# Kernel tuning notes

Hardware: AMD Instinct MI355X
Metric: run time of the kernel (lower is better)

## Reference

```python
import jax, jax.numpy as jnp
import numpy as np

NEG_SLOPE = 0.2  # PyG GATConv default LeakyReLU negative slope
NUM_GRAPHS = 256


def gat_conv(x, edge_src, edge_dst, W, att_src, att_dst, bias):
    """PyG-style GATConv. x:[N,Fin], W:[H*C,Fin], att_*:[H,C], bias:[H*C]."""
    N = x.shape[0]
    H, C = att_src.shape
    h = (x @ W.T).reshape(N, H, C)                       # [N,H,C]
    a_src = jnp.sum(h * att_src, axis=-1)                # [N,H]
    a_dst = jnp.sum(h * att_dst, axis=-1)                # [N,H]
    e = jax.nn.leaky_relu(a_src[edge_src] + a_dst[edge_dst], NEG_SLOPE)  # [E,H]
    # segment softmax over edges sharing the same destination node
    m = jax.ops.segment_max(e, edge_dst, num_segments=N)
    ex = jnp.exp(e - m[edge_dst])
    den = jax.ops.segment_sum(ex, edge_dst, num_segments=N)
    alpha = ex / (den[edge_dst] + 1e-16)                 # [E,H]
    out = jax.ops.segment_sum(h[edge_src] * alpha[..., None], edge_dst,
                              num_segments=N)            # [N,H,C]
    return out.reshape(N, H * C) + bias


def setup_inputs() -> dict:
    key = jax.random.key(0)
    ks = jax.random.split(key, 16)
    N, E, Fin = 20000, 320000, 128
    H1, C1 = 8, 64          # conv1: heads=8, hidden_dim1=64 -> concat 512
    D1 = H1 * C1            # 512
    D2 = 128                # hidden_dim2, conv2 heads=1
    OUT = 2
    s = lambda k, shp, fan: jax.random.normal(k, shp, jnp.float32) * (1.0 / np.sqrt(fan))
    x = jax.random.normal(ks[0], (N, Fin), jnp.float32)
    edge_index = jax.random.randint(ks[1], (2, E), 0, N, jnp.int32)
    batch = jnp.sort(jax.random.randint(ks[2], (N,), 0, NUM_GRAPHS, jnp.int32))
    return {
        "x": x, "edge_index": edge_index, "batch": batch,
        "W1": s(ks[3], (D1, Fin), Fin), "att_src1": s(ks[4], (H1, C1), C1),
        "att_dst1": s(ks[5], (H1, C1), C1), "b1": jnp.zeros((D1,), jnp.float32),
        "W2": s(ks[6], (D2, D1), D1), "att_src2": s(ks[7], (1, D2), D2),
        "att_dst2": s(ks[8], (1, D2), D2), "b2": jnp.zeros((D2,), jnp.float32),
        "w_attn": s(ks[9], (D2, 1), D2), "b_attn": jnp.zeros((1,), jnp.float32),
        "w_mask": s(ks[10], (D2, 1), D2), "b_mask": jnp.zeros((1,), jnp.float32),
        "W_out": s(ks[11], (OUT, D2), D2), "b_out": jnp.zeros((OUT,), jnp.float32),
    }


def reference(x, edge_index, batch, W1, att_src1, att_dst1, b1,
              W2, att_src2, att_dst2, b2, w_attn, b_attn, w_mask, b_mask,
              W_out, b_out):
    N = x.shape[0]
    loops = jnp.arange(N, dtype=edge_index.dtype)
    src = jnp.concatenate([edge_index[0], loops])  # PyG add_self_loops=True
    dst = jnp.concatenate([edge_index[1], loops])

    h = gat_conv(x, src, dst, W1, att_src1, att_dst1, b1)   # [N, 512]
    h = jax.nn.relu(h)                                      # dropout = identity (eval)
    h = gat_conv(h, src, dst, W2, att_src2, att_dst2, b2)   # [N, 128]
    h = jax.nn.relu(h)

    # attention pooling over graphs in the batch
    attn_scores = h @ w_attn + b_attn                       # [N,1]
    node_mask = jax.nn.sigmoid(h @ w_mask + b_mask)         # [N,1]
    weighted = h * (attn_scores * node_mask)                # [N,128]
    pooled = jax.ops.segment_sum(weighted, batch, num_segments=NUM_GRAPHS)
    return pooled @ W_out.T + b_out                         # [256, 2]
```

## Files before the change

kernel.cpp:

```cpp
#include <hip/hip_runtime.h>
#include <math.h>


#define NEG_SLOPE 0.2f

using bf16x8 = __attribute__((ext_vector_type(8))) __bf16;
using f32x4  = __attribute__((ext_vector_type(4))) float;

__device__ __forceinline__ ushort f2bf(float f) {
    unsigned u = __float_as_uint(f);
    unsigned r = (u + 0x7FFFu + ((u >> 16) & 1u)) >> 16;
    return (ushort)r;
}
__device__ __forceinline__ unsigned pack2(float a, float b) {
    return (unsigned)f2bf(a) | ((unsigned)f2bf(b) << 16);
}
__device__ __forceinline__ void unpack8(uint4 u, float* f) {
    f[0] = __uint_as_float(u.x << 16); f[1] = __uint_as_float(u.x & 0xFFFF0000u);
    f[2] = __uint_as_float(u.y << 16); f[3] = __uint_as_float(u.y & 0xFFFF0000u);
    f[4] = __uint_as_float(u.z << 16); f[5] = __uint_as_float(u.z & 0xFFFF0000u);
    f[6] = __uint_as_float(u.w << 16); f[7] = __uint_as_float(u.w & 0xFFFF0000u);
}
__device__ __forceinline__ void unpack4(uint2 u, float* f) {
    f[0] = __uint_as_float(u.x << 16); f[1] = __uint_as_float(u.x & 0xFFFF0000u);
    f[2] = __uint_as_float(u.y << 16); f[3] = __uint_as_float(u.y & 0xFFFF0000u);
}

__global__ __launch_bounds__(256) void cvt_bf16(const float* __restrict__ in,
                                                ushort* __restrict__ out, int n4) {
    int i = blockIdx.x * 256 + threadIdx.x;
    if (i >= n4) return;
    float4 v = ((const float4*)in)[i];
    uint2 o;
    o.x = pack2(v.x, v.y);
    o.y = pack2(v.z, v.w);
    ((uint2*)out)[i] = o;
}

__global__ __launch_bounds__(256) void prep_v(const float* __restrict__ W1,
                                              const float* __restrict__ att_s,
                                              const float* __restrict__ att_d,
                                              float* __restrict__ v_s,
                                              float* __restrict__ v_d) {
    int tid = blockIdx.x * 256 + threadIdx.x;
    int h = tid >> 7, f = tid & 127;
    float as = 0.f, ad = 0.f;
    for (int c = 0; c < 64; ++c) {
        float w = W1[(size_t)(h * 64 + c) * 128 + f];
        as += att_s[h * 64 + c] * w;
        ad += att_d[h * 64 + c] * w;
    }
    v_s[tid] = as;
    v_d[tid] = ad;
}

__global__ __launch_bounds__(256) void scoresA(const ushort* __restrict__ xb,
                                               const float* __restrict__ v_s,
                                               const float* __restrict__ v_d,
                                               float* __restrict__ a1s,
                                               float* __restrict__ a1d, int N) {
    int node = blockIdx.x * 4 + (threadIdx.x >> 6);
    if (node >= N) return;
    int lane = threadIdx.x & 63;
    int head = lane >> 3, f0 = (lane & 7) * 16;
    const uint4* xp = (const uint4*)(xb + (size_t)node * 128 + f0);
    float xv[16];
    unpack8(xp[0], xv);
    unpack8(xp[1], xv + 8);
    const float4* sp = (const float4*)(v_s + head * 128 + f0);
    const float4* dp = (const float4*)(v_d + head * 128 + f0);
    float ps = 0.f, pd = 0.f;
#pragma unroll
    for (int q = 0; q < 4; ++q) {
        float4 s4 = sp[q], d4 = dp[q];
        ps += xv[q*4+0]*s4.x + xv[q*4+1]*s4.y + xv[q*4+2]*s4.z + xv[q*4+3]*s4.w;
        pd += xv[q*4+0]*d4.x + xv[q*4+1]*d4.y + xv[q*4+2]*d4.z + xv[q*4+3]*d4.w;
    }
#pragma unroll
    for (int off = 1; off < 8; off <<= 1) {
        ps += __shfl_xor(ps, off);
        pd += __shfl_xor(pd, off);
    }
    if ((lane & 7) == 0) {
        a1s[node * 8 + head] = ps;
        a1d[node * 8 + head] = pd;
    }
}

__global__ void count_edges(const int* __restrict__ dst, int* cnt, int E) {
    int e = blockIdx.x * 256 + threadIdx.x;
    if (e < E) atomicAdd(&cnt[dst[e]], 1);
}

__global__ __launch_bounds__(1024) void scan_offsets(const int* cnt, int* row_start,
                                                     int* cursor, int N) {
    __shared__ int sm[1024];
    int t = threadIdx.x;
    int per = (N + 1023) / 1024;
    int beg = t * per;
    int end = beg + per; if (end > N) end = N;
    int sum = 0;
    for (int i = beg; i < end; ++i) sum += cnt[i];
    sm[t] = sum;
    __syncthreads();
    for (int off = 1; off < 1024; off <<= 1) {
        int add = (t >= off) ? sm[t - off] : 0;
        __syncthreads();
        sm[t] += add;
        __syncthreads();
    }
    int run = sm[t] - sum;
    for (int i = beg; i < end; ++i) {
        int c = cnt[i];
        row_start[i] = run;
        cursor[i] = run;
        run += c;
    }
    if (t == 1023) row_start[N] = run;
}

__global__ void fill_edges(const int* __restrict__ src, const int* __restrict__ dst,
                           int* cursor, int* __restrict__ srcs, int E) {
    int e = blockIdx.x * 256 + threadIdx.x;
    if (e < E) {
        int pos = atomicAdd(&cursor[dst[e]], 1);
        srcs[pos] = src[e];
    }
}

__global__ __launch_bounds__(256) void agg_x(const ushort* __restrict__ xb,
                                             const float* __restrict__ a1s,
                                             const float* __restrict__ a1d,
                                             const int* __restrict__ row_start,
                                             const int* __restrict__ srcs,
                                             ushort* __restrict__ ax, int N) {
    int node = blockIdx.x * 4 + (threadIdx.x >> 6);
    if (node >= N) return;
    int lane = threadIdx.x & 63;
    int head = lane >> 3, f0 = (lane & 7) * 16;
    int pbeg = row_start[node], pend = row_start[node + 1];
    float ad = a1d[node * 8 + head];
    float es = a1s[node * 8 + head] + ad;
    es = es > 0.f ? es : NEG_SLOPE * es;
    float ex_self = __expf(es);
    float den = ex_self;
    float acc[16];
    {
        const uint4* xp = (const uint4*)(xb + (size_t)node * 128 + f0);
        float xv[16];
        unpack8(xp[0], xv);
        unpack8(xp[1], xv + 8);
#pragma unroll
        for (int j = 0; j < 16; ++j) acc[j] = ex_self * xv[j];
    }
    for (int p = pbeg; p < pend; ++p) {
        int s = srcs[p];
        float e = a1s[s * 8 + head] + ad;
        e = e > 0.f ? e : NEG_SLOPE * e;
        float ex = __expf(e);
        den += ex;
        const uint4* xp = (const uint4*)(xb + (size_t)s * 128 + f0);
        float xv[16];
        unpack8(xp[0], xv);
        unpack8(xp[1], xv + 8);
#pragma unroll
        for (int j = 0; j < 16; ++j) acc[j] += ex * xv[j];
    }
    float rden = 1.0f / (den + 1e-16f);
    uint4 o0, o1;
    o0.x = pack2(acc[0] * rden, acc[1] * rden);
    o0.y = pack2(acc[2] * rden, acc[3] * rden);
    o0.z = pack2(acc[4] * rden, acc[5] * rden);
    o0.w = pack2(acc[6] * rden, acc[7] * rden);
    o1.x = pack2(acc[8] * rden, acc[9] * rden);
    o1.y = pack2(acc[10] * rden, acc[11] * rden);
    o1.z = pack2(acc[12] * rden, acc[13] * rden);
    o1.w = pack2(acc[14] * rden, acc[15] * rden);
    uint4* op = (uint4*)(ax + (size_t)node * 1024 + head * 128 + f0);
    op[0] = o0; op[1] = o1;
}

#define LDSB 40
__global__ __launch_bounds__(256) void gemm_grouped(const ushort* __restrict__ AX,
                                                    const ushort* __restrict__ W1b,
                                                    const float* __restrict__ b1,
                                                    ushort* __restrict__ r1,
                                                    int M) {
    __shared__ ushort As[2][128 * LDSB];
    __shared__ ushort Bs[128 * LDSB];
    int t = threadIdx.x;
    int wave = t >> 6, lane = t & 63;
    int quad = lane >> 4, l16 = lane & 15;
    int m0 = blockIdx.x * 128;
    int y = blockIdx.y;
    int wm = (wave & 1) * 64;
    int wn = (wave >> 1) * 64;
    int hsel = wn >> 6;
    int srow = t >> 1;
    int sseg = (t & 1) * 16;
    f32x4 acc[4][4] = {};
    for (int k0 = 0; k0 < 128; k0 += 32) {
        uint4 a0v0, a0v1, a1v0, a1v1, bv0, bv1;
        {
            int grow = m0 + srow;
            if (grow < M) {
                const uint4* g0 = (const uint4*)(AX + (size_t)grow * 1024 + (2 * y) * 128 + k0 + sseg);
                const uint4* g1 = (const uint4*)(AX + (size_t)grow * 1024 + (2 * y + 1) * 128 + k0 + sseg);
                a0v0 = g0[0]; a0v1 = g0[1];
                a1v0 = g1[0]; a1v1 = g1[1];
            } else {
                a0v0 = make_uint4(0, 0, 0, 0); a0v1 = a0v0; a1v0 = a0v0; a1v1 = a0v0;
            }
            const uint4* gq = (const uint4*)(W1b + (size_t)(y * 128 + srow) * 128 + k0 + sseg);
            bv0 = gq[0]; bv1 = gq[1];
        }
        __syncthreads();
        *(uint4*)&As[0][srow * LDSB + sseg]     = a0v0;
        *(uint4*)&As[0][srow * LDSB + sseg + 8] = a0v1;
        *(uint4*)&As[1][srow * LDSB + sseg]     = a1v0;
        *(uint4*)&As[1][srow * LDSB + sseg + 8] = a1v1;
        *(uint4*)&Bs[srow * LDSB + sseg]        = bv0;
        *(uint4*)&Bs[srow * LDSB + sseg + 8]    = bv1;
        __syncthreads();
        bf16x8 af[4], bf[4];
#pragma unroll
        for (int i = 0; i < 4; ++i)
            af[i] = *(const bf16x8*)&As[hsel][(wm + i * 16 + l16) * LDSB + quad * 8];
#pragma unroll
        for (int j = 0; j < 4; ++j)
            bf[j] = *(const bf16x8*)&Bs[(wn + j * 16 + l16) * LDSB + quad * 8];
#pragma unroll
        for (int i = 0; i < 4; ++i)
#pragma unroll
            for (int j = 0; j < 4; ++j)
                acc[i][j] = __builtin_amdgcn_mfma_f32_16x16x32_bf16(
                    af[i], bf[j], acc[i][j], 0, 0, 0);
    }
#pragma unroll
    for (int i = 0; i < 4; ++i) {
#pragma unroll
        for (int r = 0; r < 4; ++r) {
            int grow = m0 + wm + i * 16 + quad * 4 + r;
            if (grow < M) {
#pragma unroll
                for (int j = 0; j < 4; ++j) {
                    int gcol = y * 128 + wn + j * 16 + l16;
                    float v = fmaxf(acc[i][j][r] + b1[gcol], 0.f);
                    r1[(size_t)grow * 512 + gcol] = f2bf(v);
                }
            }
        }
    }
}

__global__ __launch_bounds__(256) void gemm_mfma(const ushort* __restrict__ A,
                                                 const ushort* __restrict__ B,
                                                 ushort* __restrict__ C,
                                                 int M, int N, int K) {
    __shared__ ushort As[128 * LDSB];
    __shared__ ushort Bs[128 * LDSB];
    int t = threadIdx.x;
    int wave = t >> 6, lane = t & 63;
    int quad = lane >> 4, l16 = lane & 15;
    int m0 = blockIdx.x * 128;
    int n0 = blockIdx.y * 128;
    int wm = (wave & 1) * 64;
    int wn = (wave >> 1) * 64;
    int srow = t >> 1;
    int sseg = (t & 1) * 16;
    f32x4 acc[4][4] = {};
    for (int k0 = 0; k0 < K; k0 += 32) {
        uint4 av0, av1, bv0, bv1;
        {
            int grow = m0 + srow;
            if (grow < M) {
                const uint4* gp = (const uint4*)(A + (size_t)grow * K + k0 + sseg);
                av0 = gp[0]; av1 = gp[1];
            } else {
                av0 = make_uint4(0, 0, 0, 0); av1 = av0;
            }
            const uint4* gq = (const uint4*)(B + (size_t)(n0 + srow) * K + k0 + sseg);
            bv0 = gq[0]; bv1 = gq[1];
        }
        __syncthreads();
        *(uint4*)&As[srow * LDSB + sseg]     = av0;
        *(uint4*)&As[srow * LDSB + sseg + 8] = av1;
        *(uint4*)&Bs[srow * LDSB + sseg]     = bv0;
        *(uint4*)&Bs[srow * LDSB + sseg + 8] = bv1;
        __syncthreads();
        bf16x8 af[4], bf[4];
#pragma unroll
        for (int i = 0; i < 4; ++i)
            af[i] = *(const bf16x8*)&As[(wm + i * 16 + l16) * LDSB + quad * 8];
#pragma unroll
        for (int j = 0; j < 4; ++j)
            bf[j] = *(const bf16x8*)&Bs[(wn + j * 16 + l16) * LDSB + quad * 8];
#pragma unroll
        for (int i = 0; i < 4; ++i)
#pragma unroll
            for (int j = 0; j < 4; ++j)
                acc[i][j] = __builtin_amdgcn_mfma_f32_16x16x32_bf16(
                    af[i], bf[j], acc[i][j], 0, 0, 0);
    }
#pragma unroll
    for (int i = 0; i < 4; ++i) {
#pragma unroll
        for (int r = 0; r < 4; ++r) {
            int grow = m0 + wm + i * 16 + quad * 4 + r;
            if (grow < M) {
#pragma unroll
                for (int j = 0; j < 4; ++j) {
                    int gcol = n0 + wn + j * 16 + l16;
                    C[(size_t)grow * N + gcol] = f2bf(acc[i][j][r]);
                }
            }
        }
    }
}

__global__ __launch_bounds__(256) void scores2(const ushort* __restrict__ h2,
                                               const float* __restrict__ att_s,
                                               const float* __restrict__ att_d,
                                               float* __restrict__ a2s,
                                               float* __restrict__ a2d, int N) {
    int node = blockIdx.x * 4 + (threadIdx.x >> 6);
    if (node >= N) return;
    int lane = threadIdx.x & 63;
    unsigned u = *(const unsigned*)(h2 + (size_t)node * 128 + lane * 2);
    float h0 = __uint_as_float(u << 16), h1v = __uint_as_float(u & 0xFFFF0000u);
    float2 s = *(const float2*)(att_s + lane * 2);
    float2 d = *(const float2*)(att_d + lane * 2);
    float ps = h0 * s.x + h1v * s.y;
    float pd = h0 * d.x + h1v * d.y;
#pragma unroll
    for (int off = 1; off < 64; off <<= 1) {
        ps += __shfl_xor(ps, off);
        pd += __shfl_xor(pd, off);
    }
    if (lane == 0) { a2s[node] = ps; a2d[node] = pd; }
}

__global__ __launch_bounds__(256) void agg2pool(const ushort* __restrict__ h2,
                                                const float* __restrict__ a2s,
                                                const float* __restrict__ a2d,
                                                const int* __restrict__ row_start,
                                                const int* __restrict__ srcs,
                                                const float* __restrict__ b2,
                                                const int* __restrict__ batch,
                                                const float* __restrict__ w_attn,
                                                const float* __restrict__ b_attn,
                                                const float* __restrict__ w_mask,
                                                const float* __restrict__ b_mask,
                                                float* pooled, int N) {
    int node = blockIdx.x * 8 + (threadIdx.x >> 5);
    if (node >= N) return;
    int sub = threadIdx.x & 31;
    int f0 = sub * 4;
    int pbeg = row_start[node], pend = row_start[node + 1];
    float ad = a2d[node];
    float es = a2s[node] + ad;
    es = es > 0.f ? es : NEG_SLOPE * es;
    float ex_self = __expf(es);
    float den = ex_self;
    float q[4];
    unpack4(*(const uint2*)(h2 + (size_t)node * 128 + f0), q);
    float acc[4];
#pragma unroll
    for (int j = 0; j < 4; ++j) acc[j] = ex_self * q[j];
    for (int p = pbeg; p < pend; ++p) {
        int s = srcs[p];
        float e = a2s[s] + ad;
        e = e > 0.f ? e : NEG_SLOPE * e;
        float ex = __expf(e);
        den += ex;
        float v[4];
        unpack4(*(const uint2*)(h2 + (size_t)s * 128 + f0), v);
#pragma unroll
        for (int j = 0; j < 4; ++j) acc[j] += ex * v[j];
    }
    float rden = 1.0f / (den + 1e-16f);
    float4 bv = *(const float4*)(b2 + f0);
    float o[4];
    o[0] = fmaxf(acc[0] * rden + bv.x, 0.f);
    o[1] = fmaxf(acc[1] * rden + bv.y, 0.f);
    o[2] = fmaxf(acc[2] * rden + bv.z, 0.f);
    o[3] = fmaxf(acc[3] * rden + bv.w, 0.f);
    float4 wa = *(const float4*)(w_attn + f0);
    float4 wm = *(const float4*)(w_mask + f0);
    float pa = o[0] * wa.x + o[1] * wa.y + o[2] * wa.z + o[3] * wa.w;
    float pm = o[0] * wm.x + o[1] * wm.y + o[2] * wm.z + o[3] * wm.w;
#pragma unroll
    for (int off = 1; off < 32; off <<= 1) {
        pa += __shfl_xor(pa, off);
        pm += __shfl_xor(pm, off);
    }
    float attn = pa + b_attn[0];
    float mask = 1.0f / (1.0f + __expf(-(pm + b_mask[0])));
    float w = attn * mask;
    int g = batch[node];
    float* pp = pooled + g * 128 + f0;
    atomicAdd(pp + 0, o[0] * w);
    atomicAdd(pp + 1, o[1] * w);
    atomicAdd(pp + 2, o[2] * w);
    atomicAdd(pp + 3, o[3] * w);
}

__global__ void final_kernel(const float* __restrict__ pooled,
                             const float* __restrict__ W_out,
                             const float* __restrict__ b_out,
                             float* __restrict__ out) {
    int tid = blockIdx.x * 256 + threadIdx.x;
    if (tid >= 512) return;
    int g = tid >> 1, o = tid & 1;
    const float* p = pooled + g * 128;
    const float* w = W_out + o * 128;
    float s = 0.f;
#pragma unroll 4
    for (int f = 0; f < 128; ++f) s += p[f] * w[f];
    out[tid] = s + b_out[o];
}

extern "C" void kernel_launch(void* const* d_in, const int* in_sizes, int n_in,
                              void* d_out, int out_size, void* d_ws, size_t ws_size,
                              hipStream_t stream) {
    const float* x        = (const float*)d_in[0];
    const int* edge_index = (const int*)d_in[1];
    const int* batch      = (const int*)d_in[2];
    const float* W1       = (const float*)d_in[3];
    const float* att_src1 = (const float*)d_in[4];
    const float* att_dst1 = (const float*)d_in[5];
    const float* b1       = (const float*)d_in[6];
    const float* W2       = (const float*)d_in[7];
    const float* att_src2 = (const float*)d_in[8];
    const float* att_dst2 = (const float*)d_in[9];
    const float* b2       = (const float*)d_in[10];
    const float* w_attn   = (const float*)d_in[11];
    const float* b_attn   = (const float*)d_in[12];
    const float* w_mask   = (const float*)d_in[13];
    const float* b_mask   = (const float*)d_in[14];
    const float* W_out    = (const float*)d_in[15];
    const float* b_out    = (const float*)d_in[16];
    float* out = (float*)d_out;

    int N = in_sizes[0] / 128;
    int E = in_sizes[1] / 2;
    const int* esrc = edge_index;
    const int* edst = edge_index + E;

    char* ws = (char*)d_ws;
    size_t off = 0;
    auto alloc = [&](size_t bytes) {
        void* p = ws + off;
        off = (off + bytes + 255) & ~(size_t)255;
        return p;
    };
    ushort* xb       = (ushort*)alloc((size_t)N * 128 * 2);
    ushort* ax       = (ushort*)alloc((size_t)N * 1024 * 2);
    ushort* r1       = (ushort*)alloc((size_t)N * 512 * 2);
    ushort* h2       = (ushort*)alloc((size_t)N * 128 * 2);
    ushort* w1b      = (ushort*)alloc((size_t)512 * 128 * 2);
    ushort* w2b      = (ushort*)alloc((size_t)128 * 512 * 2);
    float*  v_s      = (float*)alloc((size_t)8 * 128 * 4);
    float*  v_d      = (float*)alloc((size_t)8 * 128 * 4);
    float*  a1s      = (float*)alloc((size_t)N * 8 * 4);
    float*  a1d      = (float*)alloc((size_t)N * 8 * 4);
    float*  a2s      = (float*)alloc((size_t)N * 4);
    float*  a2d      = (float*)alloc((size_t)N * 4);
    int*    row_start= (int*)alloc((size_t)(N + 1) * 4);
    int*    cursor   = (int*)alloc((size_t)N * 4);
    int*    srcs     = (int*)alloc((size_t)E * 4);
    float*  pooled   = (float*)alloc((size_t)256 * 128 * 4);

    hipMemsetAsync(cursor, 0, (size_t)N * 4, stream);
    hipMemsetAsync(pooled, 0, 256 * 128 * 4, stream);

    dim3 b256(256);
    int nx4 = N * 128 / 4;
    cvt_bf16<<<(nx4 + 255) / 256, b256, 0, stream>>>(x, xb, nx4);
    cvt_bf16<<<(512 * 128 / 4 + 255) / 256, b256, 0, stream>>>(W1, w1b, 512 * 128 / 4);
    cvt_bf16<<<(128 * 512 / 4 + 255) / 256, b256, 0, stream>>>(W2, w2b, 128 * 512 / 4);
    prep_v<<<4, b256, 0, stream>>>(W1, att_src1, att_dst1, v_s, v_d);
    scoresA<<<(N + 3) / 4, b256, 0, stream>>>(xb, v_s, v_d, a1s, a1d, N);
    count_edges<<<(E + 255) / 256, b256, 0, stream>>>(edst, cursor, E);
    scan_offsets<<<1, 1024, 0, stream>>>(cursor, row_start, cursor, N);
    fill_edges<<<(E + 255) / 256, b256, 0, stream>>>(esrc, edst, cursor, srcs, E);
    agg_x<<<(N + 3) / 4, b256, 0, stream>>>(xb, a1s, a1d, row_start, srcs, ax, N);
    gemm_grouped<<<dim3((N + 127) / 128, 4), b256, 0, stream>>>(ax, w1b, b1, r1, N);
    gemm_mfma<<<dim3((N + 127) / 128, 1), b256, 0, stream>>>(r1, w2b, h2, N, 128, 512);
    scores2<<<(N + 3) / 4, b256, 0, stream>>>(h2, att_src2, att_dst2, a2s, a2d, N);
    agg2pool<<<(N + 7) / 8, b256, 0, stream>>>(h2, a2s, a2d, row_start, srcs, b2,
                                               batch, w_attn, b_attn, w_mask, b_mask,
                                               pooled, N);
    final_kernel<<<2, b256, 0, stream>>>(pooled, W_out, b_out, out);
}
```

Baseline: 330.7 us.

## Precompute per-edge attention exps and split neighbor lists across wave subgroups

Adds edge-parallel kernels that compute the exponentiated attention coefficients for both GAT layers into CSR-ordered buffers, with fill_edges now also recording destination indices. The aggregation kernels then read these precomputed values and split each node's neighbor list across four 16-lane groups, each reading a full 128-feature row once for all 8 heads, and combine the partial sums with cross-lane shuffles. The aim is to cut redundant per-head exp work and serial per-edge latency in the gather loops. In exchange it adds two launches, extra global traffic for the ex1/ex2/dsts buffers, and a large per-thread register array (64 accumulators) that may lower occupancy.

```diff
diff --git a/kernel.cpp b/kernel.cpp
--- a/kernel.cpp
+++ b/kernel.cpp
@@ -21,9 +21,9 @@
     f[4] = __uint_as_float(u.z << 16); f[5] = __uint_as_float(u.z & 0xFFFF0000u);
     f[6] = __uint_as_float(u.w << 16); f[7] = __uint_as_float(u.w & 0xFFFF0000u);
 }
-__device__ __forceinline__ void unpack4(uint2 u, float* f) {
-    f[0] = __uint_as_float(u.x << 16); f[1] = __uint_as_float(u.x & 0xFFFF0000u);
-    f[2] = __uint_as_float(u.y << 16); f[3] = __uint_as_float(u.y & 0xFFFF0000u);
+
+__device__ __forceinline__ float leaky(float e) {
+    return e > 0.f ? e : NEG_SLOPE * e;
 }
 
 __global__ __launch_bounds__(256) void cvt_bf16(const float* __restrict__ in,
@@ -120,12 +120,49 @@
 }
 
 __global__ void fill_edges(const int* __restrict__ src, const int* __restrict__ dst,
-                           int* cursor, int* __restrict__ srcs, int E) {
+                           int* cursor, int* __restrict__ srcs,
+                           int* __restrict__ dsts, int E) {
     int e = blockIdx.x * 256 + threadIdx.x;
     if (e < E) {
-        int pos = atomicAdd(&cursor[dst[e]], 1);
+        int d = dst[e];
+        int pos = atomicAdd(&cursor[d], 1);
         srcs[pos] = src[e];
-    }
+        dsts[pos] = d;
+    }
+}
+
+__global__ __launch_bounds__(256) void exp_edges1(const int* __restrict__ srcs,
+                                                  const int* __restrict__ dsts,
+                                                  const float* __restrict__ a1s,
+                                                  const float* __restrict__ a1d,
+                                                  float* __restrict__ ex1, int E) {
+    int p = blockIdx.x * 256 + threadIdx.x;
+    if (p >= E) return;
+    int s = srcs[p], d = dsts[p];
+    const float4* sp = (const float4*)(a1s + s * 8);
+    const float4* dp = (const float4*)(a1d + d * 8);
+    float4 s0 = sp[0], s1 = sp[1], d0 = dp[0], d1 = dp[1];
+    float4 o0, o1;
+    o0.x = __expf(leaky(s0.x + d0.x));
+    o0.y = __expf(leaky(s0.y + d0.y));
+    o0.z = __expf(leaky(s0.z + d0.z));
+    o0.w = __expf(leaky(s0.w + d0.w));
+    o1.x = __expf(leaky(s1.x + d1.x));
+    o1.y = __expf(leaky(s1.y + d1.y));
+    o1.z = __expf(leaky(s1.z + d1.z));
+    o1.w = __expf(leaky(s1.w + d1.w));
+    float4* op = (float4*)(ex1 + (size_t)p * 8);
+    op[0] = o0; op[1] = o1;
+}
+
+__global__ __launch_bounds__(256) void exp_edges2(const int* __restrict__ srcs,
+                                                  const int* __restrict__ dsts,
+                                                  const float* __restrict__ a2s,
+                                                  const float* __restrict__ a2d,
+                                                  float* __restrict__ ex2, int E) {
+    int p = blockIdx.x * 256 + threadIdx.x;
+    if (p >= E) return;
+    ex2[p] = __expf(leaky(a2s[srcs[p]] + a2d[dsts[p]]));
 }
 
 __global__ __launch_bounds__(256) void agg_x(const ushort* __restrict__ xb,
@@ -133,51 +170,73 @@
                                              const float* __restrict__ a1d,
                                              const int* __restrict__ row_start,
                                              const int* __restrict__ srcs,
+                                             const float* __restrict__ ex1,
                                              ushort* __restrict__ ax, int N) {
     int node = blockIdx.x * 4 + (threadIdx.x >> 6);
     if (node >= N) return;
     int lane = threadIdx.x & 63;
-    int head = lane >> 3, f0 = (lane & 7) * 16;
+    int eg = lane >> 4, fl = lane & 15;
+    int f0 = fl * 8;
     int pbeg = row_start[node], pend = row_start[node + 1];
-    float ad = a1d[node * 8 + head];
-    float es = a1s[node * 8 + head] + ad;
-    es = es > 0.f ? es : NEG_SLOPE * es;
-    float ex_self = __expf(es);
-    float den = ex_self;
-    float acc[16];
+    float acc[8][8] = {};
+    float den[8] = {};
+    for (int p = pbeg + eg; p < pend; p += 4) {
+        int s = srcs[p];
+        const float4* ep = (const float4*)(ex1 + (size_t)p * 8);
+        float4 e0 = ep[0], e1 = ep[1];
+        float ex[8] = {e0.x, e0.y, e0.z, e0.w, e1.x, e1.y, e1.z, e1.w};
+        float xv[8];
+        unpack8(*(const uint4*)(xb + (size_t)s * 128 + f0), xv);
+#pragma unroll
+        for (int h = 0; h < 8; ++h) {
+            den[h] += ex[h];
+#pragma unroll
+            for (int j = 0; j < 8; ++j) acc[h][j] += ex[h] * xv[j];
+        }
+    }
+#pragma unroll
+    for (int h = 0; h < 8; ++h) {
+        den[h] += __shfl_xor(den[h], 16);
+        den[h] += __shfl_xor(den[h], 32);
+#pragma unroll
+        for (int j = 0; j < 8; ++j) {
+            acc[h][j] += __shfl_xor(acc[h][j], 16);
+            acc[h][j] += __shfl_xor(acc[h][j], 32);
+        }
+    }
     {
-        const uint4* xp = (const uint4*)(xb + (size_t)node * 128 + f0);
-        float xv[16];
-        unpack8(xp[0], xv);
-        unpack8(xp[1], xv + 8);
-#pragma unroll
-        for (int j = 0; j < 16; ++j) acc[j] = ex_self * xv[j];
-    }
-    for (int p = pbeg; p < pend; ++p) {
-        int s = srcs[p];
-        float e = a1s[s * 8 + head] + ad;
-        e = e > 0.f ? e : NEG_SLOPE * e;
-        float ex = __expf(e);
-        den += ex;
-        const uint4* xp = (const uint4*)(xb + (size_t)s * 128 + f0);
-        float xv[16];
-        unpack8(xp[0], xv);
-        unpack8(xp[1], xv + 8);
-#pragma unroll
-        for (int j = 0; j < 16; ++j) acc[j] += ex * xv[j];
-    }
-    float rden = 1.0f / (den + 1e-16f);
-    uint4 o0, o1;
-    o0.x = pack2(acc[0] * rden, acc[1] * rden);
-    o0.y = pack2(acc[2] * rden, acc[3] * rden);
-    o0.z = pack2(acc[4] * rden, acc[5] * rden);
-    o0.w = pack2(acc[6] * rden, acc[7] * rden);
-    o1.x = pack2(acc[8] * rden, acc[9] * rden);
-    o1.y = pack2(acc[10] * rden, acc[11] * rden);
-    o1.z = pack2(acc[12] * rden, acc[13] * rden);
-    o1.w = pack2(acc[14] * rden, acc[15] * rden);
-    uint4* op = (uint4*)(ax + (size_t)node * 1024 + head * 128 + f0);
-    op[0] = o0; op[1] = o1;
+        const float4* sp = (const float4*)(a1s + node * 8);
+        const float4* dp = (const float4*)(a1d + node * 8);
+        float4 s0 = sp[0], s1 = sp[1], d0 = dp[0], d1 = dp[1];
+        float exs[8];
+        exs[0] = __expf(leaky(s0.x + d0.x));
+        exs[1] = __expf(leaky(s0.y + d0.y));
+        exs[2] = __expf(leaky(s0.z + d0.z));
+        exs[3] = __expf(leaky(s0.w + d0.w));
+        exs[4] = __expf(leaky(s1.x + d1.x));
+        exs[5] = __expf(leaky(s1.y + d1.y));
+        exs[6] = __expf(leaky(s1.z + d1.z));
+        exs[7] = __expf(leaky(s1.w + d1.w));
+        float xv[8];
+        unpack8(*(const uint4*)(xb + (size_t)node * 128 + f0), xv);
+#pragma unroll
+        for (int h = 0; h < 8; ++h) {
+            den[h] += exs[h];
+#pragma unroll
+            for (int j = 0; j < 8; ++j) acc[h][j] += exs[h] * xv[j];
+        }
+    }
+#pragma unroll
+    for (int hh = 0; hh < 2; ++hh) {
+        int h = eg * 2 + hh;
+        float rden = 1.0f / (den[h] + 1e-16f);
+        uint4 o;
+        o.x = pack2(acc[h][0] * rden, acc[h][1] * rden);
+        o.y = pack2(acc[h][2] * rden, acc[h][3] * rden);
+        o.z = pack2(acc[h][4] * rden, acc[h][5] * rden);
+        o.w = pack2(acc[h][6] * rden, acc[h][7] * rden);
+        *(uint4*)(ax + (size_t)node * 1024 + h * 128 + f0) = o;
+    }
 }
 
 #define LDSB 40
@@ -345,6 +404,7 @@
                                                 const float* __restrict__ a2d,
                                                 const int* __restrict__ row_start,
                                                 const int* __restrict__ srcs,
+                                                const float* __restrict__ ex2,
                                                 const float* __restrict__ b2,
                                                 const int* __restrict__ batch,
                                                 const float* __restrict__ w_attn,
@@ -352,57 +412,71 @@
                                                 const float* __restrict__ w_mask,
                                                 const float* __restrict__ b_mask,
                                                 float* pooled, int N) {
-    int node = blockIdx.x * 8 + (threadIdx.x >> 5);
+    int node = blockIdx.x * 4 + (threadIdx.x >> 6);
     if (node >= N) return;
-    int sub = threadIdx.x & 31;
-    int f0 = sub * 4;
+    int lane = threadIdx.x & 63;
+    int eg = lane >> 4, fl = lane & 15;
+    int f0 = fl * 8;
     int pbeg = row_start[node], pend = row_start[node + 1];
-    float ad = a2d[node];
-    float es = a2s[node] + ad;
-    es = es > 0.f ? es : NEG_SLOPE * es;
-    float ex_self = __expf(es);
-    float den = ex_self;
-    float q[4];
-    unpack4(*(const uint2*)(h2 + (size_t)node * 128 + f0), q);
-    float acc[4];
-#pragma unroll
-    for (int j = 0; j < 4; ++j) acc[j] = ex_self * q[j];
-    for (int p = pbeg; p < pend; ++p) {
+    float acc[8] = {};
+    float den = 0.f;
+    for (int p = pbeg + eg; p < pend; p += 4) {
         int s = srcs[p];
-        float e = a2s[s] + ad;
-        e = e > 0.f ? e : NEG_SLOPE * e;
-        float ex = __expf(e);
+        float ex = ex2[p];
+        float v[8];
+        unpack8(*(const uint4*)(h2 + (size_t)s * 128 + f0), v);
         den += ex;
-        float v[4];
-        unpack4(*(const uint2*)(h2 + (size_t)s * 128 + f0), v);
-#pragma unroll
-        for (int j = 0; j < 4; ++j) acc[j] += ex * v[j];
+#pragma unroll
+        for (int j = 0; j < 8; ++j) acc[j] += ex * v[j];
+    }
+    den += __shfl_xor(den, 16);
+    den += __shfl_xor(den, 32);
+#pragma unroll
+    for (int j = 0; j < 8; ++j) {
+        acc[j] += __shfl_xor(acc[j], 16);
+        acc[j] += __shfl_xor(acc[j], 32);
+    }
+    {
+        float exs = __expf(leaky(a2s[node] + a2d[node]));
+        float q[8];
+        unpack8(*(const uint4*)(h2 + (size_t)node * 128 + f0), q);
+        den += exs;
+#pragma unroll
+        for (int j = 0; j < 8; ++j) acc[j] += exs * q[j];
     }
     float rden = 1.0f / (den + 1e-16f);
-    float4 bv = *(const float4*)(b2 + f0);
-    float o[4];
-    o[0] = fmaxf(acc[0] * rden + bv.x, 0.f);
-    o[1] = fmaxf(acc[1] * rden + bv.y, 0.f);
-    o[2] = fmaxf(acc[2] * rden + bv.z, 0.f);
-    o[3] = fmaxf(acc[3] * rden + bv.w, 0.f);
-    float4 wa = *(const float4*)(w_attn + f0);
-    float4 wm = *(const float4*)(w_mask + f0);
-    float pa = o[0] * wa.x + o[1] * wa.y + o[2] * wa.z + o[3] * wa.w;
-    float pm = o[0] * wm.x + o[1] * wm.y + o[2] * wm.z + o[3] * wm.w;
-#pragma unroll
-    for (int off = 1; off < 32; off <<= 1) {
+    const float4* bp = (const float4*)(b2 + f0);
+    float4 b0 = bp[0], b1v = bp[1];
+    float o[8];
+    o[0] = fmaxf(acc[0] * rden + b0.x, 0.f);
+    o[1] = fmaxf(acc[1] * rden + b0.y, 0.f);
+    o[2] = fmaxf(acc[2] * rden + b0.z, 0.f);
+    o[3] = fmaxf(acc[3] * rden + b0.w, 0.f);
+    o[4] = fmaxf(acc[4] * rden + b1v.x, 0.f);
+    o[5] = fmaxf(acc[5] * rden + b1v.y, 0.f);
+    o[6] = fmaxf(acc[6] * rden + b1v.z, 0.f);
+    o[7] = fmaxf(acc[7] * rden + b1v.w, 0.f);
+    const float4* wap = (const float4*)(w_attn + f0);
+    const float4* wmp = (const float4*)(w_mask + f0);
+    float4 wa0 = wap[0], wa1 = wap[1], wm0 = wmp[0], wm1 = wmp[1];
+    float pa = o[0]*wa0.x + o[1]*wa0.y + o[2]*wa0.z + o[3]*wa0.w +
+               o[4]*wa1.x + o[5]*wa1.y + o[6]*wa1.z + o[7]*wa1.w;
+    float pm = o[0]*wm0.x + o[1]*wm0.y + o[2]*wm0.z + o[3]*wm0.w +
+               o[4]*wm1.x + o[5]*wm1.y + o[6]*wm1.z + o[7]*wm1.w;
+#pragma unroll
+    for (int off = 1; off < 16; off <<= 1) {
         pa += __shfl_xor(pa, off);
         pm += __shfl_xor(pm, off);
     }
     float attn = pa + b_attn[0];
     float mask = 1.0f / (1.0f + __expf(-(pm + b_mask[0])));
     float w = attn * mask;
-    int g = batch[node];
-    float* pp = pooled + g * 128 + f0;
-    atomicAdd(pp + 0, o[0] * w);
-    atomicAdd(pp + 1, o[1] * w);
-    atomicAdd(pp + 2, o[2] * w);
-    atomicAdd(pp + 3, o[3] * w);
+    if (eg == 0) {
+        int g = batch[node];
+        float* pp = pooled + g * 128 + f0;
+#pragma unroll
+        for (int j = 0; j < 8; ++j) atomicAdd(pp + j, o[j] * w);
+    }
 }
 
 __global__ void final_kernel(const float* __restrict__ pooled,
@@ -469,6 +543,9 @@
     int*    row_start= (int*)alloc((size_t)(N + 1) * 4);
     int*    cursor   = (int*)alloc((size_t)N * 4);
     int*    srcs     = (int*)alloc((size_t)E * 4);
+    int*    dsts     = (int*)alloc((size_t)E * 4);
+    float*  ex1      = (float*)alloc((size_t)E * 8 * 4);
+    float*  ex2      = (float*)alloc((size_t)E * 4);
     float*  pooled   = (float*)alloc((size_t)256 * 128 * 4);
 
     hipMemsetAsync(cursor, 0, (size_t)N * 4, stream);
@@ -483,12 +560,14 @@
     scoresA<<<(N + 3) / 4, b256, 0, stream>>>(xb, v_s, v_d, a1s, a1d, N);
     count_edges<<<(E + 255) / 256, b256, 0, stream>>>(edst, cursor, E);
     scan_offsets<<<1, 1024, 0, stream>>>(cursor, row_start, cursor, N);
-    fill_edges<<<(E + 255) / 256, b256, 0, stream>>>(esrc, edst, cursor, srcs, E);
-    agg_x<<<(N + 3) / 4, b256, 0, stream>>>(xb, a1s, a1d, row_start, srcs, ax, N);
+    fill_edges<<<(E + 255) / 256, b256, 0, stream>>>(esrc, edst, cursor, srcs, dsts, E);
+    exp_edges1<<<(E + 255) / 256, b256, 0, stream>>>(srcs, dsts, a1s, a1d, ex1, E);
+    agg_x<<<(N + 3) / 4, b256, 0, stream>>>(xb, a1s, a1d, row_start, srcs, ex1, ax, N);
     gemm_grouped<<<dim3((N + 127) / 128, 4), b256, 0, stream>>>(ax, w1b, b1, r1, N);
     gemm_mfma<<<dim3((N + 127) / 128, 1), b256, 0, stream>>>(r1, w2b, h2, N, 128, 512);
     scores2<<<(N + 3) / 4, b256, 0, stream>>>(h2, att_src2, att_dst2, a2s, a2d, N);
-    agg2pool<<<(N + 7) / 8, b256, 0, stream>>>(h2, a2s, a2d, row_start, srcs, b2,
+    exp_edges2<<<(E + 255) / 256, b256, 0, stream>>>(srcs, dsts, a2s, a2d, ex2, E);
+    agg2pool<<<(N + 3) / 4, b256, 0, stream>>>(h2, a2s, a2d, row_start, srcs, ex2, b2,
                                                batch, w_attn, b_attn, w_mask, b_mask,
                                                pooled, N);
     final_kernel<<<2, b256, 0, stream>>>(pooled, W_out, b_out, out);
```

Result: slower. 567.3 us (+71.6%).
